# Optimization experiments

Hardware: AMD Instinct MI355X
Metric: run time of the kernel (lower is better)

Reference implementation:

```python
import jax, jax.numpy as jnp
import numpy as np

VOCAB = 32000
HID = 1024
BATCH = 8
SEQ = 512


def setup_inputs() -> dict:
    key = jax.random.key(0)
    k1, k2, k3, k4 = jax.random.split(key, 4)
    scale = 1.0 / np.sqrt(HID)
    return {
        "batched_sequence_ids": jax.random.randint(k1, (BATCH, SEQ), 0, VOCAB, dtype=jnp.int32),
        "w_out": jax.random.normal(k2, (HID, VOCAB), dtype=jnp.float32) * scale,
        "b_out": jnp.zeros((VOCAB,), dtype=jnp.float32),
        "W_ih": jax.random.normal(k3, (HID, 4 * HID), dtype=jnp.float32) * scale,
        "W_hh": jax.random.normal(k4, (HID, 4 * HID), dtype=jnp.float32) * scale,
        "b_lstm": jnp.zeros((4 * HID,), dtype=jnp.float32),
    }


def _lstm_scan(x_gates, W_hh):
    # x_gates: [B, S, 4H] = precomputed input contribution + bias
    B = x_gates.shape[0]
    H = W_hh.shape[0]
    h0 = jnp.zeros((B, H), dtype=x_gates.dtype)
    c0 = jnp.zeros((B, H), dtype=x_gates.dtype)

    def step(carry, xg_t):
        h, c = carry
        gates = xg_t + h @ W_hh  # [B, 4H]
        i, f, g, o = jnp.split(gates, 4, axis=-1)
        i = jax.nn.sigmoid(i)
        f = jax.nn.sigmoid(f)
        g = jnp.tanh(g)
        o = jax.nn.sigmoid(o)
        c_new = f * c + i * g
        h_new = o * jnp.tanh(c_new)
        return (h_new, c_new), h_new

    # scan over time axis: move S to leading dim
    (_, _), hs = jax.lax.scan(step, (h0, c0), jnp.swapaxes(x_gates, 0, 1))
    return jnp.swapaxes(hs, 0, 1)  # [B, S, H]


def reference(batched_sequence_ids, w_out, b_out, W_ih, W_hh, b_lstm):
    # weight-tied embedding lookup: w_out is [H, V]; emb = w_out[:, ids].T
    emb = jnp.take(w_out.T, batched_sequence_ids, axis=0)  # [B, S, H]
    # precompute input-to-gate contribution for all timesteps in one GEMM
    x_gates = jnp.einsum('bsh,hg->bsg', emb, W_ih) + b_lstm  # [B, S, 4H]
    hs = _lstm_scan(x_gates, W_hh)  # [B, S, H]
    logits = jnp.einsum('bsh,hv->bsv', hs, w_out) + b_out  # [B, S, V]
    return logits
```

## Files before the change

### kernel.cpp

```cpp
#include <hip/hip_runtime.h>
#include <math.h>

#define VOCAB 32000
#define HID   1024
#define BATCH 8
#define SEQ   512
#define GD    (4*HID)
#define ROWS  (BATCH*SEQ)

typedef __attribute__((ext_vector_type(8))) short short8;
typedef __attribute__((ext_vector_type(4))) float f32x4;

__device__ __forceinline__ float hi_f32(float x) {
    return __uint_as_float(__float_as_uint(x) & 0xFFFF0000u);
}
__device__ __forceinline__ unsigned pack_pair(float x) {
    unsigned hb = __float_as_uint(x) & 0xFFFF0000u;
    float lo = x - __uint_as_float(hb);
    return hb | (__float_as_uint(lo) >> 16);
}
__device__ __forceinline__ unsigned pack_hi2(float x, float y) {
    return (__float_as_uint(x) >> 16) | (__float_as_uint(y) & 0xFFFF0000u);
}

__device__ __forceinline__ void gload16(const void* g, void* l) {
    __builtin_amdgcn_global_load_lds(
        (__attribute__((address_space(1))) void*)g,
        (__attribute__((address_space(3))) void*)l, 16, 0, 0);
}

__global__ __launch_bounds__(256) void k_gather_split(const int* __restrict__ ids,
                                                      const float* __restrict__ w_out,
                                                      unsigned short* __restrict__ emb_hi,
                                                      unsigned short* __restrict__ emb_lo)
{
    int row = blockIdx.x;
    int id  = ids[row];
    const float* src = w_out + id;
    for (int h = threadIdx.x; h < HID; h += 256) {
        float v  = src[(size_t)h * VOCAB];
        float lo = v - hi_f32(v);
        emb_hi[(size_t)row*HID + h] = (unsigned short)(__float_as_uint(v)  >> 16);
        emb_lo[(size_t)row*HID + h] = (unsigned short)(__float_as_uint(lo) >> 16);
    }
}

__global__ __launch_bounds__(256) void k_transsplit(const float* __restrict__ W,
                                                    unsigned short* __restrict__ hiT,
                                                    unsigned short* __restrict__ loT,
                                                    int N)
{
    __shared__ float tile[32][33];
    int tx = threadIdx.x, ty = threadIdx.y;
    int x = blockIdx.x*32 + tx;
    int y = blockIdx.y*32 + ty;
    #pragma unroll
    for (int i = 0; i < 32; i += 8)
        tile[ty + i][tx] = W[(size_t)(y + i)*N + x];
    __syncthreads();
    int n = blockIdx.x*32 + ty;
    int k = blockIdx.y*32 + tx;
    #pragma unroll
    for (int i = 0; i < 32; i += 8) {
        float v  = tile[tx][ty + i];
        float lo = v - hi_f32(v);
        hiT[(size_t)(n + i)*HID + k] = (unsigned short)(__float_as_uint(v)  >> 16);
        loT[(size_t)(n + i)*HID + k] = (unsigned short)(__float_as_uint(lo) >> 16);
    }
}

__global__ __launch_bounds__(256) void k_split_f32(const float* __restrict__ src,
                                                   unsigned short* __restrict__ hi,
                                                   unsigned short* __restrict__ lo,
                                                   long n4)
{
    long i0 = (long)blockIdx.x * 256 + threadIdx.x;
    long stride = (long)gridDim.x * 256;
    for (long i = i0; i < n4; i += stride) {
        float4 v = ((const float4*)src)[i];
        unsigned h0 = __float_as_uint(v.x) >> 16, h1 = __float_as_uint(v.y) >> 16;
        unsigned h2 = __float_as_uint(v.z) >> 16, h3 = __float_as_uint(v.w) >> 16;
        unsigned l0 = __float_as_uint(v.x - hi_f32(v.x)) >> 16;
        unsigned l1 = __float_as_uint(v.y - hi_f32(v.y)) >> 16;
        unsigned l2 = __float_as_uint(v.z - hi_f32(v.z)) >> 16;
        unsigned l3 = __float_as_uint(v.w - hi_f32(v.w)) >> 16;
        ((uint2*)hi)[i] = make_uint2(h0 | (h1 << 16), h2 | (h3 << 16));
        ((uint2*)lo)[i] = make_uint2(l0 | (l1 << 16), l2 | (l3 << 16));
    }
}

__global__ __launch_bounds__(256) void k_zero16(uint4* __restrict__ p, long n16)
{
    long i = (long)blockIdx.x * 256 + threadIdx.x;
    if (i < n16) p[i] = make_uint4(0u, 0u, 0u, 0u);
}

#define GBM 128
#define GBN 128
#define GBK 32

__global__ __launch_bounds__(256) void k_gemm_fast(
    const unsigned short* __restrict__ Ah,  const unsigned short* __restrict__ Al,
    const unsigned short* __restrict__ BhT, const unsigned short* __restrict__ BlT,
    const float* __restrict__ bias, float* __restrict__ C,
    int M, int N, int K)
{
    __shared__ __align__(16) unsigned short lds[4][4096];

    const int tid  = threadIdx.x;
    const int lane = tid & 63;
    const int wid  = tid >> 6;
    const int wm = wid >> 1, wn = wid & 1;
    const int l15 = lane & 15, l4 = lane >> 4;
    const int brow = blockIdx.y * GBM;
    const int bcol = blockIdx.x * GBN;

    const int lhi  = lane >> 3;
    const int c8   = (lane & 7) ^ lhi;
    const int koff = (c8 & 3) * 8;
    const int r0   = 32*wid + 2*lhi + (c8 >> 2);
    const int r1   = r0 + 16;
    const size_t a0 = (size_t)(brow + r0)*K + koff;
    const size_t a1 = (size_t)(brow + r1)*K + koff;
    const size_t b0 = (size_t)(bcol + r0)*K + koff;
    const size_t b1 = (size_t)(bcol + r1)*K + koff;
    char* lbase = (char*)&lds[0][0];
    const int cb0 = wid*2048, cb1 = wid*2048 + 1024;

    const int ra = wm*64 + l15;
    const int ga = ra >> 1;
    const int abyte = ga*128 + (((((ra & 1) << 2) | l4) ^ (ga & 7)) << 4);
    const int rb = wn*64 + l15;
    const int gb = rb >> 1;
    const int bbyte = gb*128 + (((((rb & 1) << 2) | l4) ^ (gb & 7)) << 4);

    f32x4 acc[4][4] = {};

    for (int k0 = 0; k0 < K; k0 += GBK) {
        gload16(Ah  + a0 + k0, lbase         + cb0);
        gload16(Ah  + a1 + k0, lbase         + cb1);
        gload16(Al  + a0 + k0, lbase + 8192  + cb0);
        gload16(Al  + a1 + k0, lbase + 8192  + cb1);
        gload16(BhT + b0 + k0, lbase + 16384 + cb0);
        gload16(BhT + b1 + k0, lbase + 16384 + cb1);
        gload16(BlT + b0 + k0, lbase + 24576 + cb0);
        gload16(BlT + b1 + k0, lbase + 24576 + cb1);
        __syncthreads();

        short8 ah[4], al[4], bh[4], bl[4];
        #pragma unroll
        for (int m = 0; m < 4; ++m) {
            ah[m] = *(const short8*)(lbase         + abyte + m*1024);
            al[m] = *(const short8*)(lbase + 8192  + abyte + m*1024);
        }
        #pragma unroll
        for (int n = 0; n < 4; ++n) {
            bh[n] = *(const short8*)(lbase + 16384 + bbyte + n*1024);
            bl[n] = *(const short8*)(lbase + 24576 + bbyte + n*1024);
        }
        #pragma unroll
        for (int n = 0; n < 4; ++n)
            #pragma unroll
            for (int m = 0; m < 4; ++m) {
                acc[m][n] = __builtin_amdgcn_mfma_f32_16x16x32_bf16(ah[m], bh[n], acc[m][n], 0, 0, 0);
                acc[m][n] = __builtin_amdgcn_mfma_f32_16x16x32_bf16(ah[m], bl[n], acc[m][n], 0, 0, 0);
                acc[m][n] = __builtin_amdgcn_mfma_f32_16x16x32_bf16(al[m], bh[n], acc[m][n], 0, 0, 0);
            }
        __syncthreads();
    }

    #pragma unroll
    for (int n = 0; n < 4; ++n) {
        int col = bcol + wn*64 + n*16 + l15;
        float bv = bias[col];
        #pragma unroll
        for (int m = 0; m < 4; ++m) {
            int rbs = brow + wm*64 + m*16 + l4*4;
            #pragma unroll
            for (int r = 0; r < 4; ++r)
                C[(size_t)(rbs + r)*N + col] = acc[m][n][r] + bv;
        }
    }
}

__global__ __launch_bounds__(256) void k_gemm_mfma(const float* __restrict__ A,
                                                   const float* __restrict__ B,
                                                   const float* __restrict__ bias,
                                                   float* __restrict__ C,
                                                   int M, int N, int K)
{
    __shared__ unsigned short As_hi[GBM][40];
    __shared__ unsigned short As_lo[GBM][40];
    __shared__ unsigned int   Bs[GBK][130];

    int tid  = threadIdx.x;
    int brow = blockIdx.y * GBM;
    int bcol = blockIdx.x * GBN;

    int lane = tid & 63;
    int wid  = tid >> 6;
    int wm   = wid >> 1;
    int wn   = wid & 1;
    int l15  = lane & 15;
    int l4   = lane >> 4;

    int a_m = tid >> 3;
    int a_c = tid & 7;
    int b_k = tid >> 5;
    int b_n = tid & 31;

    f32x4 acc[4][4] = {};

    for (int k0 = 0; k0 < K; k0 += GBK) {
        #pragma unroll
        for (int p = 0; p < 4; ++p) {
            int r = a_m + p*32;
            float4 v = *(const float4*)(A + (size_t)(brow + r)*K + k0 + a_c*4);
            unsigned h0 = pack_hi2(v.x, v.y);
            unsigned h1 = pack_hi2(v.z, v.w);
            float lx = v.x - hi_f32(v.x);
            float ly = v.y - hi_f32(v.y);
            float lz = v.z - hi_f32(v.z);
            float lw = v.w - hi_f32(v.w);
            unsigned l0 = pack_hi2(lx, ly);
            unsigned l1 = pack_hi2(lz, lw);
            *(uint2*)&As_hi[r][a_c*4] = make_uint2(h0, h1);
            *(uint2*)&As_lo[r][a_c*4] = make_uint2(l0, l1);
        }
        #pragma unroll
        for (int p = 0; p < 4; ++p) {
            int kk = b_k + p*8;
            float4 v = *(const float4*)(B + (size_t)(k0 + kk)*N + bcol + b_n*4);
            unsigned w0 = pack_pair(v.x);
            unsigned w1 = pack_pair(v.y);
            unsigned w2 = pack_pair(v.z);
            unsigned w3 = pack_pair(v.w);
            *(uint2*)&Bs[kk][b_n*4]     = make_uint2(w0, w1);
            *(uint2*)&Bs[kk][b_n*4 + 2] = make_uint2(w2, w3);
        }
        __syncthreads();

        short8 ah[4], al[4];
        #pragma unroll
        for (int m = 0; m < 4; ++m) {
            int r = wm*64 + m*16 + l15;
            ah[m] = *(const short8*)&As_hi[r][l4*8];
            al[m] = *(const short8*)&As_lo[r][l4*8];
        }

        #pragma unroll
        for (int n = 0; n < 4; ++n) {
            int col = wn*64 + n*16 + l15;
            unsigned w[8];
            #pragma unroll
            for (int j = 0; j < 8; ++j)
                w[j] = Bs[l4*8 + j][col];
            union { short8 v; unsigned d[4]; } bh, bl;
            #pragma unroll
            for (int d = 0; d < 4; ++d) {
                bh.d[d] = (w[2*d] >> 16)      | (w[2*d+1] & 0xFFFF0000u);
                bl.d[d] = (w[2*d] & 0xFFFFu)  | (w[2*d+1] << 16);
            }
            #pragma unroll
            for (int m = 0; m < 4; ++m) {
                acc[m][n] = __builtin_amdgcn_mfma_f32_16x16x32_bf16(ah[m], bh.v, acc[m][n], 0, 0, 0);
                acc[m][n] = __builtin_amdgcn_mfma_f32_16x16x32_bf16(ah[m], bl.v, acc[m][n], 0, 0, 0);
                acc[m][n] = __builtin_amdgcn_mfma_f32_16x16x32_bf16(al[m], bh.v, acc[m][n], 0, 0, 0);
            }
        }
        __syncthreads();
    }

    #pragma unroll
    for (int n = 0; n < 4; ++n) {
        int col = bcol + wn*64 + n*16 + l15;
        float bv = bias[col];
        #pragma unroll
        for (int m = 0; m < 4; ++m) {
            int rb = brow + wm*64 + m*16 + l4*4;
            #pragma unroll
            for (int r = 0; r < 4; ++r)
                C[(size_t)(rb + r)*N + col] = acc[m][n][r] + bv;
        }
    }
}

__global__ __launch_bounds__(256) void k_lstm_step_mfma(
    const float* __restrict__ xg,
    const unsigned short* __restrict__ WhT_hi,
    const unsigned short* __restrict__ WhT_lo,
    const unsigned short* __restrict__ hp_hi,
    const unsigned short* __restrict__ hp_lo,
    unsigned short* __restrict__ hn_hi,
    unsigned short* __restrict__ hn_lo,
    float* __restrict__ c_state,
    float* __restrict__ hs,
    int t)
{
    __shared__ float g_part[4][16][16];

    const int tid  = threadIdx.x;
    const int lane = tid & 63;
    const int kq   = tid >> 6;
    const int l15  = lane & 15;
    const int l4   = lane >> 4;
    const int j0   = blockIdx.x * 4;
    const int bcol = (l15 >> 2)*HID + j0 + (l15 & 3);

    float xv0 = 0, xv1 = 0, xv2 = 0, xv3 = 0, cv = 0;
    const int tb = tid & 7;
    const int tj = (tid >> 3) & 3;
    if (tid < 32) {
        int jc = j0 + tj;
        size_t xbase = ((size_t)tb*SEQ + t)*GD + jc;
        xv0 = xg[xbase];
        xv1 = xg[xbase + HID];
        xv2 = xg[xbase + 2*HID];
        xv3 = xg[xbase + 3*HID];
        cv  = (t > 0) ? c_state[(size_t)tb*HID + jc] : 0.0f;
    }

    if (t > 0) {
        const int krow = l4*8;
        const unsigned short* wh = WhT_hi + (size_t)bcol*HID + krow;
        const unsigned short* wl = WhT_lo + (size_t)bcol*HID + krow;
        const unsigned short* ah = hp_hi  + (size_t)l15*HID + krow;
        const unsigned short* al = hp_lo  + (size_t)l15*HID + krow;

        f32x4 acc0 = {}, acc1 = {};
        #pragma unroll
        for (int ks = 0; ks < 8; ks += 2) {
            int ka = kq*256 + ks*32;
            int kb = ka + 32;
            short8 Ah0 = *(const short8*)(ah + ka);
            short8 Al0 = *(const short8*)(al + ka);
            short8 Bh0 = *(const short8*)(wh + ka);
            short8 Bl0 = *(const short8*)(wl + ka);
            short8 Ah1 = *(const short8*)(ah + kb);
            short8 Al1 = *(const short8*)(al + kb);
            short8 Bh1 = *(const short8*)(wh + kb);
            short8 Bl1 = *(const short8*)(wl + kb);
            acc0 = __builtin_amdgcn_mfma_f32_16x16x32_bf16(Ah0, Bh0, acc0, 0, 0, 0);
            acc1 = __builtin_amdgcn_mfma_f32_16x16x32_bf16(Ah1, Bh1, acc1, 0, 0, 0);
            acc0 = __builtin_amdgcn_mfma_f32_16x16x32_bf16(Ah0, Bl0, acc0, 0, 0, 0);
            acc1 = __builtin_amdgcn_mfma_f32_16x16x32_bf16(Ah1, Bl1, acc1, 0, 0, 0);
            acc0 = __builtin_amdgcn_mfma_f32_16x16x32_bf16(Al0, Bh0, acc0, 0, 0, 0);
            acc1 = __builtin_amdgcn_mfma_f32_16x16x32_bf16(Al1, Bh1, acc1, 0, 0, 0);
        }
        f32x4 acc = acc0 + acc1;
        *(f32x4*)&g_part[kq][l15][l4*4] = acc;
    }
    __syncthreads();

    if (tid < 32) {
        int jc = j0 + tj;
        float sv[4];
        #pragma unroll
        for (int g = 0; g < 4; ++g) {
            int colL = g*4 + tj;
            sv[g] = (t > 0) ? (g_part[0][colL][tb] + g_part[1][colL][tb]
                             + g_part[2][colL][tb] + g_part[3][colL][tb])
                            : 0.0f;
        }
        float iv = sv[0] + xv0;
        float fv = sv[1] + xv1;
        float gv = sv[2] + xv2;
        float ov = sv[3] + xv3;
        iv = 1.0f / (1.0f + expf(-iv));
        fv = 1.0f / (1.0f + expf(-fv));
        gv = tanhf(gv);
        ov = 1.0f / (1.0f + expf(-ov));
        float cn = fv*cv + iv*gv;
        float hn = ov * tanhf(cn);
        c_state[(size_t)tb*HID + jc] = cn;
        hs[((size_t)tb*SEQ + t)*HID + jc] = hn;
        unsigned hb = __float_as_uint(hn) & 0xFFFF0000u;
        hn_hi[(size_t)tb*HID + jc] = (unsigned short)(hb >> 16);
        hn_lo[(size_t)tb*HID + jc] =
            (unsigned short)(__float_as_uint(hn - __uint_as_float(hb)) >> 16);
    }
}

extern "C" void kernel_launch(void* const* d_in, const int* in_sizes, int n_in,
                              void* d_out, int out_size, void* d_ws, size_t ws_size,
                              hipStream_t stream)
{
    const int*   ids    = (const int*)  d_in[0];
    const float* w_out  = (const float*)d_in[1];
    const float* b_out  = (const float*)d_in[2];
    const float* W_ih   = (const float*)d_in[3];
    const float* W_hh   = (const float*)d_in[4];
    const float* b_lstm = (const float*)d_in[5];
    float* out = (float*)d_out;

    char* ob = (char*)d_out;
    unsigned short* emb_hi  = (unsigned short*)(ob);
    unsigned short* emb_lo  = (unsigned short*)(ob + 8388608);
    unsigned short* whh_hiT = (unsigned short*)(ob + 16777216);
    unsigned short* whh_loT = (unsigned short*)(ob + 25165824);
    float*          xg      = (float*)(ob + 33554432);
    float*          cstate  = (float*)(ob + 100663296);
    unsigned short* wih_hiT = (unsigned short*)(ob + 100696064);
    unsigned short* wih_loT = (unsigned short*)(ob + 109084672);
    float*          hs_dout = (float*)(ob + 117473280);
    unsigned short* hb0_hi  = (unsigned short*)(ob + 134250496);
    unsigned short* hb0_lo  = (unsigned short*)(ob + 134283264);
    unsigned short* hb1_hi  = (unsigned short*)(ob + 134316032);
    unsigned short* hb1_lo  = (unsigned short*)(ob + 134348800);

    char* wb = (char*)d_ws;
    const size_t NEED = 147849216ull;
    const bool big_ws = (ws_size >= NEED);
    unsigned short* hs_hi  = (unsigned short*)(wb);
    unsigned short* hs_lo  = (unsigned short*)(wb + 8388608);
    unsigned short* wo_hiT = (unsigned short*)(wb + 16777216);
    unsigned short* wo_loT = (unsigned short*)(wb + 82313216);
    float* hs = big_ws ? hs_dout : (float*)wb;

    k_gather_split<<<ROWS, 256, 0, stream>>>(ids, w_out, emb_hi, emb_lo);

    k_transsplit<<<dim3(GD/32, HID/32), dim3(32, 8), 0, stream>>>(
        W_hh, whh_hiT, whh_loT, GD);

    k_transsplit<<<dim3(GD/32, HID/32), dim3(32, 8), 0, stream>>>(
        W_ih, wih_hiT, wih_loT, GD);

    k_zero16<<<32, 256, 0, stream>>>((uint4*)hb0_hi, 8192);

    k_gemm_fast<<<dim3(GD/GBN, ROWS/GBM), 256, 0, stream>>>(
        emb_hi, emb_lo, wih_hiT, wih_loT, b_lstm, xg, ROWS, GD, HID);

    for (int t = 0; t < SEQ; ++t) {
        unsigned short* rd_hi = (t & 1) ? hb0_hi : hb1_hi;
        unsigned short* rd_lo = (t & 1) ? hb0_lo : hb1_lo;
        unsigned short* wr_hi = (t & 1) ? hb1_hi : hb0_hi;
        unsigned short* wr_lo = (t & 1) ? hb1_lo : hb0_lo;
        k_lstm_step_mfma<<<HID/4, 256, 0, stream>>>(
            xg, whh_hiT, whh_loT, rd_hi, rd_lo, wr_hi, wr_lo, cstate, hs, t);
    }

    if (big_ws) {
        k_transsplit<<<dim3(VOCAB/32, HID/32), dim3(32, 8), 0, stream>>>(
            w_out, wo_hiT, wo_loT, VOCAB);
        k_split_f32<<<1024, 256, 0, stream>>>(hs, hs_hi, hs_lo, (long)ROWS*HID/4);
        k_gemm_fast<<<dim3(VOCAB/GBN, ROWS/GBM), 256, 0, stream>>>(
            hs_hi, hs_lo, wo_hiT, wo_loT, b_out, out, ROWS, VOCAB, HID);
    } else {
        k_gemm_mfma<<<dim3(VOCAB/GBN, ROWS/GBM), 256, 0, stream>>>(
            hs, w_out, b_out, out, ROWS, VOCAB, HID);
    }
}
```

Baseline: 4.671 ms.

## Restructure LSTM step to 64 blocks of 512 threads and fuse hs splitting

The recurrent step kernel now runs 64 blocks of 512 threads instead of 256 blocks of 256. Each block owns 16 hidden units, and each wave handles one gate and half of K, with the 16-row MFMA tile covering batch rows 0-7 twice via l15&7. The step writes the bf16 hi/lo split of h directly into the hs buffers, so the separate split pass before the output GEMM and the zeroing kernel are removed. Fewer blocks mean less launch and scheduling cost per step, but each wave does twice the K work, so per-step latency could rise. Half of the MFMA rows are now redundant.

```diff
diff --git a/kernel.cpp b/kernel.cpp
--- a/kernel.cpp
+++ b/kernel.cpp
@@ -69,32 +69,6 @@
     }
 }
 
-__global__ __launch_bounds__(256) void k_split_f32(const float* __restrict__ src,
-                                                   unsigned short* __restrict__ hi,
-                                                   unsigned short* __restrict__ lo,
-                                                   long n4)
-{
-    long i0 = (long)blockIdx.x * 256 + threadIdx.x;
-    long stride = (long)gridDim.x * 256;
-    for (long i = i0; i < n4; i += stride) {
-        float4 v = ((const float4*)src)[i];
-        unsigned h0 = __float_as_uint(v.x) >> 16, h1 = __float_as_uint(v.y) >> 16;
-        unsigned h2 = __float_as_uint(v.z) >> 16, h3 = __float_as_uint(v.w) >> 16;
-        unsigned l0 = __float_as_uint(v.x - hi_f32(v.x)) >> 16;
-        unsigned l1 = __float_as_uint(v.y - hi_f32(v.y)) >> 16;
-        unsigned l2 = __float_as_uint(v.z - hi_f32(v.z)) >> 16;
-        unsigned l3 = __float_as_uint(v.w - hi_f32(v.w)) >> 16;
-        ((uint2*)hi)[i] = make_uint2(h0 | (h1 << 16), h2 | (h3 << 16));
-        ((uint2*)lo)[i] = make_uint2(l0 | (l1 << 16), l2 | (l3 << 16));
-    }
-}
-
-__global__ __launch_bounds__(256) void k_zero16(uint4* __restrict__ p, long n16)
-{
-    long i = (long)blockIdx.x * 256 + threadIdx.x;
-    if (i < n16) p[i] = make_uint4(0u, 0u, 0u, 0u);
-}
-
 #define GBM 128
 #define GBN 128
 #define GBK 32
@@ -285,61 +259,61 @@
     }
 }
 
-__global__ __launch_bounds__(256) void k_lstm_step_mfma(
+__global__ __launch_bounds__(512) void k_lstm_step3(
     const float* __restrict__ xg,
     const unsigned short* __restrict__ WhT_hi,
     const unsigned short* __restrict__ WhT_lo,
-    const unsigned short* __restrict__ hp_hi,
-    const unsigned short* __restrict__ hp_lo,
-    unsigned short* __restrict__ hn_hi,
-    unsigned short* __restrict__ hn_lo,
+    const unsigned short* __restrict__ pp_rd_hi,
+    const unsigned short* __restrict__ pp_rd_lo,
+    unsigned short* __restrict__ pp_wr_hi,
+    unsigned short* __restrict__ pp_wr_lo,
     float* __restrict__ c_state,
-    float* __restrict__ hs,
+    float* __restrict__ hs_f32,
+    unsigned short* __restrict__ hs_hi,
+    unsigned short* __restrict__ hs_lo,
     int t)
 {
-    __shared__ float g_part[4][16][16];
+    __shared__ float g_sm[2][4][16][20];
 
     const int tid  = threadIdx.x;
     const int lane = tid & 63;
-    const int kq   = tid >> 6;
+    const int wv   = tid >> 6;
+    const int gate = wv & 3;
+    const int kh   = wv >> 2;
     const int l15  = lane & 15;
     const int l4   = lane >> 4;
-    const int j0   = blockIdx.x * 4;
-    const int bcol = (l15 >> 2)*HID + j0 + (l15 & 3);
+    const int j0   = blockIdx.x * 16;
 
     float xv0 = 0, xv1 = 0, xv2 = 0, xv3 = 0, cv = 0;
     const int tb = tid & 7;
-    const int tj = (tid >> 3) & 3;
-    if (tid < 32) {
-        int jc = j0 + tj;
-        size_t xbase = ((size_t)tb*SEQ + t)*GD + jc;
-        xv0 = xg[xbase];
-        xv1 = xg[xbase + HID];
-        xv2 = xg[xbase + 2*HID];
-        xv3 = xg[xbase + 3*HID];
-        cv  = (t > 0) ? c_state[(size_t)tb*HID + jc] : 0.0f;
+    const int tj = tid >> 3;
+    if (tid < 128) {
+        size_t xb = ((size_t)tb*SEQ + t)*GD + j0 + tj;
+        xv0 = xg[xb];
+        xv1 = xg[xb + HID];
+        xv2 = xg[xb + 2*HID];
+        xv3 = xg[xb + 3*HID];
+        cv  = (t > 0) ? c_state[(size_t)tb*HID + j0 + tj] : 0.0f;
     }
 
     if (t > 0) {
-        const int krow = l4*8;
-        const unsigned short* wh = WhT_hi + (size_t)bcol*HID + krow;
-        const unsigned short* wl = WhT_lo + (size_t)bcol*HID + krow;
-        const unsigned short* ah = hp_hi  + (size_t)l15*HID + krow;
-        const unsigned short* al = hp_lo  + (size_t)l15*HID + krow;
+        const int kbase = kh*512 + l4*8;
+        const unsigned short* wh = WhT_hi + (size_t)(gate*HID + j0 + l15)*HID + kbase;
+        const unsigned short* wl = WhT_lo + (size_t)(gate*HID + j0 + l15)*HID + kbase;
+        const unsigned short* ah = pp_rd_hi + (size_t)(l15 & 7)*HID + kbase;
+        const unsigned short* al = pp_rd_lo + (size_t)(l15 & 7)*HID + kbase;
 
         f32x4 acc0 = {}, acc1 = {};
         #pragma unroll
-        for (int ks = 0; ks < 8; ks += 2) {
-            int ka = kq*256 + ks*32;
-            int kb = ka + 32;
-            short8 Ah0 = *(const short8*)(ah + ka);
-            short8 Al0 = *(const short8*)(al + ka);
-            short8 Bh0 = *(const short8*)(wh + ka);
-            short8 Bl0 = *(const short8*)(wl + ka);
-            short8 Ah1 = *(const short8*)(ah + kb);
-            short8 Al1 = *(const short8*)(al + kb);
-            short8 Bh1 = *(const short8*)(wh + kb);
-            short8 Bl1 = *(const short8*)(wl + kb);
+        for (int ks = 0; ks < 16; ks += 2) {
+            short8 Ah0 = *(const short8*)(ah + ks*32);
+            short8 Al0 = *(const short8*)(al + ks*32);
+            short8 Bh0 = *(const short8*)(wh + ks*32);
+            short8 Bl0 = *(const short8*)(wl + ks*32);
+            short8 Ah1 = *(const short8*)(ah + (ks+1)*32);
+            short8 Al1 = *(const short8*)(al + (ks+1)*32);
+            short8 Bh1 = *(const short8*)(wh + (ks+1)*32);
+            short8 Bl1 = *(const short8*)(wl + (ks+1)*32);
             acc0 = __builtin_amdgcn_mfma_f32_16x16x32_bf16(Ah0, Bh0, acc0, 0, 0, 0);
             acc1 = __builtin_amdgcn_mfma_f32_16x16x32_bf16(Ah1, Bh1, acc1, 0, 0, 0);
             acc0 = __builtin_amdgcn_mfma_f32_16x16x32_bf16(Ah0, Bl0, acc0, 0, 0, 0);
@@ -348,36 +322,40 @@
             acc1 = __builtin_amdgcn_mfma_f32_16x16x32_bf16(Al1, Bh1, acc1, 0, 0, 0);
         }
         f32x4 acc = acc0 + acc1;
-        *(f32x4*)&g_part[kq][l15][l4*4] = acc;
+        *(f32x4*)&g_sm[kh][gate][l15][l4*4] = acc;
     }
     __syncthreads();
 
-    if (tid < 32) {
-        int jc = j0 + tj;
-        float sv[4];
-        #pragma unroll
-        for (int g = 0; g < 4; ++g) {
-            int colL = g*4 + tj;
-            sv[g] = (t > 0) ? (g_part[0][colL][tb] + g_part[1][colL][tb]
-                             + g_part[2][colL][tb] + g_part[3][colL][tb])
-                            : 0.0f;
-        }
-        float iv = sv[0] + xv0;
-        float fv = sv[1] + xv1;
-        float gv = sv[2] + xv2;
-        float ov = sv[3] + xv3;
+    if (tid < 128) {
+        float s0 = 0, s1 = 0, s2 = 0, s3 = 0;
+        if (t > 0) {
+            s0 = g_sm[0][0][tj][tb] + g_sm[1][0][tj][tb];
+            s1 = g_sm[0][1][tj][tb] + g_sm[1][1][tj][tb];
+            s2 = g_sm[0][2][tj][tb] + g_sm[1][2][tj][tb];
+            s3 = g_sm[0][3][tj][tb] + g_sm[1][3][tj][tb];
+        }
+        float iv = s0 + xv0;
+        float fv = s1 + xv1;
+        float gv = s2 + xv2;
+        float ov = s3 + xv3;
         iv = 1.0f / (1.0f + expf(-iv));
         fv = 1.0f / (1.0f + expf(-fv));
         gv = tanhf(gv);
         ov = 1.0f / (1.0f + expf(-ov));
         float cn = fv*cv + iv*gv;
         float hn = ov * tanhf(cn);
+        int jc = j0 + tj;
         c_state[(size_t)tb*HID + jc] = cn;
-        hs[((size_t)tb*SEQ + t)*HID + jc] = hn;
+        size_t row = (size_t)tb*SEQ + t;
+        hs_f32[row*HID + jc] = hn;
         unsigned hb = __float_as_uint(hn) & 0xFFFF0000u;
-        hn_hi[(size_t)tb*HID + jc] = (unsigned short)(hb >> 16);
-        hn_lo[(size_t)tb*HID + jc] =
+        unsigned short hu = (unsigned short)(hb >> 16);
+        unsigned short lu =
             (unsigned short)(__float_as_uint(hn - __uint_as_float(hb)) >> 16);
+        hs_hi[row*HID + jc] = hu;
+        hs_lo[row*HID + jc] = lu;
+        pp_wr_hi[(size_t)tb*HID + jc] = hu;
+        pp_wr_lo[(size_t)tb*HID + jc] = lu;
     }
 }
 
@@ -400,13 +378,15 @@
     unsigned short* whh_loT = (unsigned short*)(ob + 25165824);
     float*          xg      = (float*)(ob + 33554432);
     float*          cstate  = (float*)(ob + 100663296);
-    unsigned short* wih_hiT = (unsigned short*)(ob + 100696064);
-    unsigned short* wih_loT = (unsigned short*)(ob + 109084672);
-    float*          hs_dout = (float*)(ob + 117473280);
-    unsigned short* hb0_hi  = (unsigned short*)(ob + 134250496);
-    unsigned short* hb0_lo  = (unsigned short*)(ob + 134283264);
-    unsigned short* hb1_hi  = (unsigned short*)(ob + 134316032);
-    unsigned short* hb1_lo  = (unsigned short*)(ob + 134348800);
+    unsigned short* pp0_hi  = (unsigned short*)(ob + 100696064);
+    unsigned short* pp0_lo  = (unsigned short*)(ob + 100712448);
+    unsigned short* pp1_hi  = (unsigned short*)(ob + 100728832);
+    unsigned short* pp1_lo  = (unsigned short*)(ob + 100745216);
+    unsigned short* wih_hiT = (unsigned short*)(ob + 100761600);
+    unsigned short* wih_loT = (unsigned short*)(ob + 109150208);
+    float*          hs_dout = (float*)(ob + 117538816);
+    unsigned short* dum_hi  = (unsigned short*)(ob + 134316032);
+    unsigned short* dum_lo  = (unsigned short*)(ob + 142704640);
 
     char* wb = (char*)d_ws;
     const size_t NEED = 147849216ull;
@@ -415,7 +395,9 @@
     unsigned short* hs_lo  = (unsigned short*)(wb + 8388608);
     unsigned short* wo_hiT = (unsigned short*)(wb + 16777216);
     unsigned short* wo_loT = (unsigned short*)(wb + 82313216);
-    float* hs = big_ws ? hs_dout : (float*)wb;
+    float* hs_f32 = big_ws ? hs_dout : (float*)wb;
+    unsigned short* hsh = big_ws ? hs_hi : dum_hi;
+    unsigned short* hsl = big_ws ? hs_lo : dum_lo;
 
     k_gather_split<<<ROWS, 256, 0, stream>>>(ids, w_out, emb_hi, emb_lo);
 
@@ -425,28 +407,26 @@
     k_transsplit<<<dim3(GD/32, HID/32), dim3(32, 8), 0, stream>>>(
         W_ih, wih_hiT, wih_loT, GD);
 
-    k_zero16<<<32, 256, 0, stream>>>((uint4*)hb0_hi, 8192);
-
     k_gemm_fast<<<dim3(GD/GBN, ROWS/GBM), 256, 0, stream>>>(
         emb_hi, emb_lo, wih_hiT, wih_loT, b_lstm, xg, ROWS, GD, HID);
 
     for (int t = 0; t < SEQ; ++t) {
-        unsigned short* rd_hi = (t & 1) ? hb0_hi : hb1_hi;
-        unsigned short* rd_lo = (t & 1) ? hb0_lo : hb1_lo;
-        unsigned short* wr_hi = (t & 1) ? hb1_hi : hb0_hi;
-        unsigned short* wr_lo = (t & 1) ? hb1_lo : hb0_lo;
-        k_lstm_step_mfma<<<HID/4, 256, 0, stream>>>(
-            xg, whh_hiT, whh_loT, rd_hi, rd_lo, wr_hi, wr_lo, cstate, hs, t);
+        unsigned short* rd_hi = (t & 1) ? pp0_hi : pp1_hi;
+        unsigned short* rd_lo = (t & 1) ? pp0_lo : pp1_lo;
+        unsigned short* wr_hi = (t & 1) ? pp1_hi : pp0_hi;
+        unsigned short* wr_lo = (t & 1) ? pp1_lo : pp0_lo;
+        k_lstm_step3<<<64, 512, 0, stream>>>(
+            xg, whh_hiT, whh_loT, rd_hi, rd_lo, wr_hi, wr_lo,
+            cstate, hs_f32, hsh, hsl, t);
     }
 
     if (big_ws) {
         k_transsplit<<<dim3(VOCAB/32, HID/32), dim3(32, 8), 0, stream>>>(
             w_out, wo_hiT, wo_loT, VOCAB);
-        k_split_f32<<<1024, 256, 0, stream>>>(hs, hs_hi, hs_lo, (long)ROWS*HID/4);
         k_gemm_fast<<<dim3(VOCAB/GBN, ROWS/GBM), 256, 0, stream>>>(
             hs_hi, hs_lo, wo_hiT, wo_loT, b_out, out, ROWS, VOCAB, HID);
     } else {
         k_gemm_mfma<<<dim3(VOCAB/GBN, ROWS/GBM), 256, 0, stream>>>(
-            hs, w_out, b_out, out, ROWS, VOCAB, HID);
-    }
-}
+            hs_f32, w_out, b_out, out, ROWS, VOCAB, HID);
+    }
+}
```

New measurement: 9.989 ms. +113.8%, slower.
